# Optimization experiments

Measured on AMD Instinct MI355X. Metric: run time of the kernel, lower is better.

Reference implementation:

```python
import jax, jax.numpy as jnp
import numpy as np

B, T, H = 16, 2048, 1024

def setup_inputs() -> dict:
    key = jax.random.key(0)
    k1, k2, k3, k4 = jax.random.split(key, 4)
    stdv = 1.0 / np.sqrt(H)
    return {
        "hidden": jax.random.normal(k1, (B, H), dtype=jnp.float32),
        "encoder_outputs": jax.random.normal(k2, (B, T, 2 * H), dtype=jnp.float32),
        "W": jax.random.normal(k3, (H, 3 * H), dtype=jnp.float32) * stdv,  # nn.Linear(3H, H) weight
        "b": jnp.zeros((H,), dtype=jnp.float32),
        "v": jax.random.normal(k4, (H,), dtype=jnp.float32) * stdv,
    }

def reference(hidden, encoder_outputs, W, b, v):
    # hidden: (B,H); encoder_outputs: (B,T,2H)
    Bsz, Tlen, _ = encoder_outputs.shape
    Hrep = jnp.broadcast_to(hidden[:, None, :], (Bsz, Tlen, hidden.shape[-1]))  # (B,T,H)
    cat = jnp.concatenate([Hrep, encoder_outputs], axis=2)                      # (B,T,3H)
    energy = jnp.tanh(jnp.einsum('btk,hk->bth', cat, W) + b)                    # (B,T,H)
    scores = jnp.einsum('bth,h->bt', energy, v)[:, None, :]                     # (B,1,T), == bmm(v, energy^T)
    return jax.nn.softmax(scores, axis=2)
```

## Files before the change

### kernel.cpp

```cpp
#include <hip/hip_runtime.h>
#include <cstdint>

#define B_SZ 16
#define T_SZ 2048
#define H_SZ 1024
#define K_SZ 2048
#define M_SZ (B_SZ * T_SZ)

#define BM 128
#define BN 128
#define BK 64
#define LDK 72
#define KTILES (K_SZ / BK)

#define FBM 64
#define FBK 64

typedef _Float16 half8_t __attribute__((ext_vector_type(8)));
typedef _Float16 half4_t __attribute__((ext_vector_type(4)));
typedef float float4_t __attribute__((ext_vector_type(4)));

__global__ __launch_bounds__(256) void cvt_w2_kernel(
    const float* __restrict__ W, _Float16* __restrict__ dst) {
    int idx8 = blockIdx.x * 256 + threadIdx.x;
    int n = idx8 >> 8, k = (idx8 & 255) * 8;
    const float* src = W + (size_t)n * 3072 + H_SZ + k;
    float4_t a = *(const float4_t*)(src);
    float4_t b = *(const float4_t*)(src + 4);
    half8_t h;
    h[0] = (_Float16)a[0]; h[1] = (_Float16)a[1];
    h[2] = (_Float16)a[2]; h[3] = (_Float16)a[3];
    h[4] = (_Float16)b[0]; h[5] = (_Float16)b[1];
    h[6] = (_Float16)b[2]; h[7] = (_Float16)b[3];
    int nblk = n >> 4, m16 = n & 15;
    int kblk = k >> 5, quad = (k >> 3) & 3;
    size_t di = (((size_t)nblk * 64 + kblk) * 64 + quad * 16 + m16) * 8;
    *(half8_t*)(dst + di) = h;
}

__global__ __launch_bounds__(256) void hpart_kernel(
    const float* __restrict__ hidden, const float* __restrict__ W,
    const float* __restrict__ bias, float* __restrict__ hpart) {
    int wave = (blockIdx.x * 256 + threadIdx.x) >> 6;
    int lane = threadIdx.x & 63;
    int b = wave >> 10;
    int h = wave & 1023;
    const float* wrow = W + (size_t)h * 3072;
    const float* hrow = hidden + b * H_SZ;
    int k0 = lane * 16;
    float acc = 0.f;
#pragma unroll
    for (int j = 0; j < 4; ++j) {
        float4_t wv = *(const float4_t*)(wrow + k0 + j * 4);
        float4_t hv = *(const float4_t*)(hrow + k0 + j * 4);
        acc += wv[0] * hv[0] + wv[1] * hv[1] + wv[2] * hv[2] + wv[3] * hv[3];
    }
#pragma unroll
    for (int off = 32; off >= 1; off >>= 1) acc += __shfl_xor(acc, off, 64);
    if (lane == 0) hpart[b * H_SZ + h] = acc + bias[h];
}

__global__ __launch_bounds__(1024) void fused_attn_kernel(
    const float* __restrict__ enc, const _Float16* __restrict__ Bp,
    const float* __restrict__ hpart, const float* __restrict__ v,
    float* __restrict__ scores) {
    __shared__ __align__(16) _Float16 Af[2][FBM * FBK];
    __shared__ float hp_s[H_SZ];
    __shared__ float v_s[H_SZ];
    __shared__ float sred[8][FBM];

    const int tid = threadIdx.x;
    const int lane = tid & 63;
    const int w = tid >> 6;
    const int wn = w & 7;
    const int wmg = w >> 3;
    const int m16 = lane & 15, quad = lane >> 4;

    const int blockM = blockIdx.x;
    const int batch = blockM >> 5;

    hp_s[tid] = hpart[batch * H_SZ + tid];
    v_s[tid] = v[tid];

    float4_t acc[2][8];
#pragma unroll
    for (int i = 0; i < 2; ++i)
#pragma unroll
        for (int j = 0; j < 8; ++j) acc[i][j] = (float4_t){0.f, 0.f, 0.f, 0.f};

    const int arow = tid >> 4;
    const int acq = tid & 15;
    const float* Aptr = enc + (size_t)(blockM * FBM + arow) * K_SZ + acq * 4;
    const int wbyte = arow * 128 + ((((acq >> 1) ^ (arow & 7)) << 4) | ((acq & 1) * 8));
    char* AfB = (char*)Af;

    int fb[2][2];
#pragma unroll
    for (int tm = 0; tm < 2; ++tm) {
        int r = wmg * 32 + tm * 16 + m16;
#pragma unroll
        for (int ks = 0; ks < 2; ++ks)
            fb[tm][ks] = r * 128 + (((ks * 4 + quad) ^ (r & 7)) << 4);
    }

    const _Float16* Bfr = Bp + ((size_t)(wn * 8) * 64 * 64 + lane) * 8;

    {
        float4_t av = *(const float4_t*)(Aptr);
        half4_t h;
        h[0] = (_Float16)av[0]; h[1] = (_Float16)av[1];
        h[2] = (_Float16)av[2]; h[3] = (_Float16)av[3];
        *(half4_t*)(AfB + wbyte) = h;
    }
    __syncthreads();

    int cur = 0;
    for (int kt = 0; kt < K_SZ / FBK; ++kt) {
        float4_t av;
        if (kt < K_SZ / FBK - 1) av = *(const float4_t*)(Aptr + (kt + 1) * FBK);
#pragma unroll
        for (int ks = 0; ks < 2; ++ks) {
            half8_t af0 = *(const half8_t*)(AfB + cur * 8192 + fb[0][ks]);
            half8_t af1 = *(const half8_t*)(AfB + cur * 8192 + fb[1][ks]);
            const _Float16* bk = Bfr + (size_t)(kt * 2 + ks) * 512;
#pragma unroll
            for (int g = 0; g < 2; ++g) {
                half8_t bf0 = *(const half8_t*)(bk + (size_t)(g * 4 + 0) * 32768);
                half8_t bf1 = *(const half8_t*)(bk + (size_t)(g * 4 + 1) * 32768);
                half8_t bf2 = *(const half8_t*)(bk + (size_t)(g * 4 + 2) * 32768);
                half8_t bf3 = *(const half8_t*)(bk + (size_t)(g * 4 + 3) * 32768);
                __builtin_amdgcn_s_setprio(1);
                acc[0][g * 4 + 0] = __builtin_amdgcn_mfma_f32_16x16x32_f16(af0, bf0, acc[0][g * 4 + 0], 0, 0, 0);
                acc[1][g * 4 + 0] = __builtin_amdgcn_mfma_f32_16x16x32_f16(af1, bf0, acc[1][g * 4 + 0], 0, 0, 0);
                acc[0][g * 4 + 1] = __builtin_amdgcn_mfma_f32_16x16x32_f16(af0, bf1, acc[0][g * 4 + 1], 0, 0, 0);
                acc[1][g * 4 + 1] = __builtin_amdgcn_mfma_f32_16x16x32_f16(af1, bf1, acc[1][g * 4 + 1], 0, 0, 0);
                acc[0][g * 4 + 2] = __builtin_amdgcn_mfma_f32_16x16x32_f16(af0, bf2, acc[0][g * 4 + 2], 0, 0, 0);
                acc[1][g * 4 + 2] = __builtin_amdgcn_mfma_f32_16x16x32_f16(af1, bf2, acc[1][g * 4 + 2], 0, 0, 0);
                acc[0][g * 4 + 3] = __builtin_amdgcn_mfma_f32_16x16x32_f16(af0, bf3, acc[0][g * 4 + 3], 0, 0, 0);
                acc[1][g * 4 + 3] = __builtin_amdgcn_mfma_f32_16x16x32_f16(af1, bf3, acc[1][g * 4 + 3], 0, 0, 0);
                __builtin_amdgcn_s_setprio(0);
            }
        }
        if (kt < K_SZ / FBK - 1) {
            half4_t h;
            h[0] = (_Float16)av[0]; h[1] = (_Float16)av[1];
            h[2] = (_Float16)av[2]; h[3] = (_Float16)av[3];
            *(half4_t*)(AfB + (cur ^ 1) * 8192 + wbyte) = h;
        }
        __syncthreads();
        cur ^= 1;
    }

#pragma unroll
    for (int tm = 0; tm < 2; ++tm) {
        float s0 = 0.f, s1 = 0.f, s2 = 0.f, s3 = 0.f;
#pragma unroll
        for (int tn = 0; tn < 8; ++tn) {
            int nl = wn * 128 + tn * 16 + m16;
            float hpv = hp_s[nl];
            float vv = v_s[nl];
            s0 += tanhf(acc[tm][tn][0] + hpv) * vv;
            s1 += tanhf(acc[tm][tn][1] + hpv) * vv;
            s2 += tanhf(acc[tm][tn][2] + hpv) * vv;
            s3 += tanhf(acc[tm][tn][3] + hpv) * vv;
        }
#pragma unroll
        for (int off = 1; off < 16; off <<= 1) {
            s0 += __shfl_xor(s0, off, 64);
            s1 += __shfl_xor(s1, off, 64);
            s2 += __shfl_xor(s2, off, 64);
            s3 += __shfl_xor(s3, off, 64);
        }
        if (m16 == 0) {
            int rl = wmg * 32 + tm * 16 + quad * 4;
            sred[wn][rl + 0] = s0;
            sred[wn][rl + 1] = s1;
            sred[wn][rl + 2] = s2;
            sred[wn][rl + 3] = s3;
        }
    }
    __syncthreads();
    if (tid < FBM) {
        float t = 0.f;
#pragma unroll
        for (int i = 0; i < 8; ++i) t += sred[i][tid];
        scores[(size_t)blockM * FBM + tid] = t;
    }
}

__global__ __launch_bounds__(256) void softmax1_kernel(
    const float* __restrict__ scores, float* __restrict__ out) {
    __shared__ float red[256];
    const int b = blockIdx.x;
    const int tid = threadIdx.x;
    float sc[8];
    float mymax = -1e30f;
#pragma unroll
    for (int i = 0; i < 8; ++i) {
        float s = scores[b * T_SZ + i * 256 + tid];
        sc[i] = s;
        mymax = fmaxf(mymax, s);
    }
    red[tid] = mymax;
    __syncthreads();
    for (int off = 128; off >= 1; off >>= 1) {
        if (tid < off) red[tid] = fmaxf(red[tid], red[tid + off]);
        __syncthreads();
    }
    float mx = red[0];
    __syncthreads();
    float mysum = 0.f;
#pragma unroll
    for (int i = 0; i < 8; ++i) {
        sc[i] = expf(sc[i] - mx);
        mysum += sc[i];
    }
    red[tid] = mysum;
    __syncthreads();
    for (int off = 128; off >= 1; off >>= 1) {
        if (tid < off) red[tid] += red[tid + off];
        __syncthreads();
    }
    float inv = 1.0f / red[0];
#pragma unroll
    for (int i = 0; i < 8; ++i) out[b * T_SZ + i * 256 + tid] = sc[i] * inv;
}

__global__ __launch_bounds__(256, 2) void attn_gemm_kernel(
    const float* __restrict__ enc, const float* __restrict__ W,
    const float* __restrict__ hpart, const float* __restrict__ v,
    float* __restrict__ partial) {
    __shared__ _Float16 Afs[BM * LDK];
    __shared__ _Float16 Bfs[BN * LDK];
    __shared__ float hp_s[BN];
    __shared__ float v_s[BN];

    const int bidx = blockIdx.x;
    const int blockN = bidx & 7;
    const int blockM = bidx >> 3;
    const int tid = threadIdx.x;
    const int lane = tid & 63;
    const int w = tid >> 6;
    const int wm = w & 1, wn = w >> 1;
    const int m16 = lane & 15, quad = lane >> 4;

    const int n0 = blockN * BN;
    const int batch = blockM >> 4;

    if (tid < BN) {
        hp_s[tid] = hpart[batch * H_SZ + n0 + tid];
        v_s[tid] = v[n0 + tid];
    }

    float4_t acc[4][4];
#pragma unroll
    for (int i = 0; i < 4; ++i)
#pragma unroll
        for (int j = 0; j < 4; ++j) acc[i][j] = (float4_t){0.f, 0.f, 0.f, 0.f};

    const float* Abase = enc + (size_t)(blockM * BM) * K_SZ;
    const float* Bbase = W + (size_t)n0 * 3072 + H_SZ;

    for (int kt = 0; kt < KTILES; ++kt) {
        __syncthreads();
        const float* Asrc0 = Abase + kt * BK;
#pragma unroll
        for (int i = 0; i < 4; ++i) {
            int f8 = i * 256 + tid;
            int r = f8 >> 3, c8 = f8 & 7;
            const float* src = Asrc0 + (size_t)r * K_SZ + c8 * 8;
            float4_t lo = *(const float4_t*)(src);
            float4_t hi = *(const float4_t*)(src + 4);
            half8_t hv;
            hv[0] = (_Float16)lo[0]; hv[1] = (_Float16)lo[1];
            hv[2] = (_Float16)lo[2]; hv[3] = (_Float16)lo[3];
            hv[4] = (_Float16)hi[0]; hv[5] = (_Float16)hi[1];
            hv[6] = (_Float16)hi[2]; hv[7] = (_Float16)hi[3];
            *(half8_t*)&Afs[r * LDK + c8 * 8] = hv;
        }
        const float* Bsrc0 = Bbase + kt * BK;
#pragma unroll
        for (int i = 0; i < 4; ++i) {
            int f8 = i * 256 + tid;
            int r = f8 >> 3, c8 = f8 & 7;
            const float* src = Bsrc0 + (size_t)r * 3072 + c8 * 8;
            float4_t lo = *(const float4_t*)(src);
            float4_t hi = *(const float4_t*)(src + 4);
            half8_t hv;
            hv[0] = (_Float16)lo[0]; hv[1] = (_Float16)lo[1];
            hv[2] = (_Float16)lo[2]; hv[3] = (_Float16)lo[3];
            hv[4] = (_Float16)hi[0]; hv[5] = (_Float16)hi[1];
            hv[6] = (_Float16)hi[2]; hv[7] = (_Float16)hi[3];
            *(half8_t*)&Bfs[r * LDK + c8 * 8] = hv;
        }
        __syncthreads();
#pragma unroll
        for (int ks = 0; ks < 2; ++ks) {
            half8_t afrag[4], bfrag[4];
#pragma unroll
            for (int tm = 0; tm < 4; ++tm)
                afrag[tm] = *(const half8_t*)&Afs[(wm * 64 + tm * 16 + m16) * LDK + ks * 32 + quad * 8];
#pragma unroll
            for (int tn = 0; tn < 4; ++tn)
                bfrag[tn] = *(const half8_t*)&Bfs[(wn * 64 + tn * 16 + m16) * LDK + ks * 32 + quad * 8];
#pragma unroll
            for (int tm = 0; tm < 4; ++tm)
#pragma unroll
                for (int tn = 0; tn < 4; ++tn)
                    acc[tm][tn] = __builtin_amdgcn_mfma_f32_16x16x32_f16(
                        afrag[tm], bfrag[tn], acc[tm][tn], 0, 0, 0);
        }
    }

    const int slice = blockN * 2 + wn;
#pragma unroll
    for (int tm = 0; tm < 4; ++tm) {
        float s0 = 0.f, s1 = 0.f, s2 = 0.f, s3 = 0.f;
#pragma unroll
        for (int tn = 0; tn < 4; ++tn) {
            int nl = wn * 64 + tn * 16 + m16;
            float hpv = hp_s[nl];
            float vv = v_s[nl];
            s0 += tanhf(acc[tm][tn][0] + hpv) * vv;
            s1 += tanhf(acc[tm][tn][1] + hpv) * vv;
            s2 += tanhf(acc[tm][tn][2] + hpv) * vv;
            s3 += tanhf(acc[tm][tn][3] + hpv) * vv;
        }
#pragma unroll
        for (int off = 1; off < 16; off <<= 1) {
            s0 += __shfl_xor(s0, off, 64);
            s1 += __shfl_xor(s1, off, 64);
            s2 += __shfl_xor(s2, off, 64);
            s3 += __shfl_xor(s3, off, 64);
        }
        if (m16 == 0) {
            int gm = blockM * BM + wm * 64 + tm * 16 + quad * 4;
            float* dst = partial + (size_t)slice * M_SZ + gm;
            dst[0] = s0; dst[1] = s1; dst[2] = s2; dst[3] = s3;
        }
    }
}

__global__ __launch_bounds__(256) void softmax_kernel(
    const float* __restrict__ partial, float* __restrict__ out) {
    __shared__ float red[256];
    const int b = blockIdx.x;
    const int tid = threadIdx.x;
    float sc[8];
    float mymax = -1e30f;
#pragma unroll
    for (int i = 0; i < 8; ++i) {
        int t = i * 256 + tid;
        float s = 0.f;
#pragma unroll
        for (int sl = 0; sl < 16; ++sl) s += partial[(size_t)sl * M_SZ + b * T_SZ + t];
        sc[i] = s;
        mymax = fmaxf(mymax, s);
    }
    red[tid] = mymax;
    __syncthreads();
    for (int off = 128; off >= 1; off >>= 1) {
        if (tid < off) red[tid] = fmaxf(red[tid], red[tid + off]);
        __syncthreads();
    }
    float mx = red[0];
    __syncthreads();
    float mysum = 0.f;
#pragma unroll
    for (int i = 0; i < 8; ++i) {
        sc[i] = expf(sc[i] - mx);
        mysum += sc[i];
    }
    red[tid] = mysum;
    __syncthreads();
    for (int off = 128; off >= 1; off >>= 1) {
        if (tid < off) red[tid] += red[tid + off];
        __syncthreads();
    }
    float inv = 1.0f / red[0];
#pragma unroll
    for (int i = 0; i < 8; ++i) out[b * T_SZ + i * 256 + tid] = sc[i] * inv;
}

extern "C" void kernel_launch(void* const* d_in, const int* in_sizes, int n_in,
                              void* d_out, int out_size, void* d_ws, size_t ws_size,
                              hipStream_t stream) {
    const float* hidden = (const float*)d_in[0];
    const float* enc    = (const float*)d_in[1];
    const float* W      = (const float*)d_in[2];
    const float* bias   = (const float*)d_in[3];
    const float* v      = (const float*)d_in[4];
    float* out = (float*)d_out;

    float* hpart  = (float*)d_ws;
    float* scores = hpart + B_SZ * H_SZ;
    _Float16* w2h = (_Float16*)(scores + M_SZ);
    const size_t need = (size_t)((char*)(w2h + (size_t)H_SZ * K_SZ) - (char*)d_ws);

    hipLaunchKernelGGL(hpart_kernel, dim3(4096), dim3(256), 0, stream,
                       hidden, W, bias, hpart);
    if (ws_size >= need) {
        hipLaunchKernelGGL(cvt_w2_kernel, dim3(1024), dim3(256), 0, stream, W, w2h);
        hipLaunchKernelGGL(fused_attn_kernel, dim3(M_SZ / FBM), dim3(1024), 0, stream,
                           enc, w2h, hpart, v, scores);
        hipLaunchKernelGGL(softmax1_kernel, dim3(B_SZ), dim3(256), 0, stream,
                           scores, out);
    } else {
        float* partial = scores;
        hipLaunchKernelGGL(attn_gemm_kernel, dim3(2048), dim3(256), 0, stream,
                           enc, W, hpart, v, partial);
        hipLaunchKernelGGL(softmax_kernel, dim3(B_SZ), dim3(256), 0, stream,
                           partial, out);
    }
}
```

Before: 556.4 us.

## Stage W tiles in LDS via direct global-to-LDS loads with 512-thread blocks

The fused GEMM kernel now uses 512 threads (8 waves), and each wave computes a 64x128 tile instead of 32x128. Pre-converted fp16 W fragments are staged into double-buffered LDS with global_load_lds, replacing per-wave direct global loads. The K step shrinks to 32, and encoder rows are read with nontemporal loads. The aim is to cut redundant global/L2 traffic for W and to raise MFMA density per fragment load, at the cost of 128KB of LDS, more accumulator registers, and one barrier per smaller K step.

```diff
diff --git a/kernel.cpp b/kernel.cpp
--- a/kernel.cpp
+++ b/kernel.cpp
@@ -14,11 +14,18 @@
 #define KTILES (K_SZ / BK)
 
 #define FBM 64
-#define FBK 64
+#define FBK 32
+#define NSTEPS (K_SZ / FBK)
 
 typedef _Float16 half8_t __attribute__((ext_vector_type(8)));
 typedef _Float16 half4_t __attribute__((ext_vector_type(4)));
 typedef float float4_t __attribute__((ext_vector_type(4)));
+
+__device__ __forceinline__ void glds16(const _Float16* g, _Float16* l) {
+    __builtin_amdgcn_global_load_lds(
+        (const __attribute__((address_space(1))) void*)g,
+        (__attribute__((address_space(3))) void*)l, 16, 0, 0);
+}
 
 __global__ __launch_bounds__(256) void cvt_w2_kernel(
     const float* __restrict__ W, _Float16* __restrict__ dst) {
@@ -60,109 +67,112 @@
     if (lane == 0) hpart[b * H_SZ + h] = acc + bias[h];
 }
 
-__global__ __launch_bounds__(1024) void fused_attn_kernel(
+__global__ __launch_bounds__(512, 2) void fused2_attn_kernel(
     const float* __restrict__ enc, const _Float16* __restrict__ Bp,
     const float* __restrict__ hpart, const float* __restrict__ v,
     float* __restrict__ scores) {
-    __shared__ __align__(16) _Float16 Af[2][FBM * FBK];
-    __shared__ float hp_s[H_SZ];
-    __shared__ float v_s[H_SZ];
-    __shared__ float sred[8][FBM];
+    __shared__ __align__(16) _Float16 Als[2][FBM * FBK];
+    __shared__ __align__(16) _Float16 Bls[2][64 * 512];
 
     const int tid = threadIdx.x;
     const int lane = tid & 63;
     const int w = tid >> 6;
-    const int wn = w & 7;
-    const int wmg = w >> 3;
     const int m16 = lane & 15, quad = lane >> 4;
 
     const int blockM = blockIdx.x;
     const int batch = blockM >> 5;
 
-    hp_s[tid] = hpart[batch * H_SZ + tid];
-    v_s[tid] = v[tid];
-
-    float4_t acc[2][8];
-#pragma unroll
-    for (int i = 0; i < 2; ++i)
+    const int arow = tid >> 3;
+    const int ac8 = tid & 7;
+    const float* Ap = enc + (size_t)(blockM * FBM + arow) * K_SZ + ac8 * 4;
+    const int awbyte = arow * 64 +
+        ((((ac8 >> 1) ^ ((arow >> 1) & 3)) << 4) | ((ac8 & 1) << 3));
+
+    int afb[4];
+#pragma unroll
+    for (int tm = 0; tm < 4; ++tm) {
+        int r = tm * 16 + m16;
+        afb[tm] = r * 64 + ((quad ^ ((r >> 1) & 3)) << 4);
+    }
+
+    const _Float16* Bg = Bp + ((size_t)(w * 8) * 64) * 512 + lane * 8;
+
+    float4_t acc[4][8];
+#pragma unroll
+    for (int i = 0; i < 4; ++i)
 #pragma unroll
         for (int j = 0; j < 8; ++j) acc[i][j] = (float4_t){0.f, 0.f, 0.f, 0.f};
 
-    const int arow = tid >> 4;
-    const int acq = tid & 15;
-    const float* Aptr = enc + (size_t)(blockM * FBM + arow) * K_SZ + acq * 4;
-    const int wbyte = arow * 128 + ((((acq >> 1) ^ (arow & 7)) << 4) | ((acq & 1) * 8));
-    char* AfB = (char*)Af;
-
-    int fb[2][2];
-#pragma unroll
-    for (int tm = 0; tm < 2; ++tm) {
-        int r = wmg * 32 + tm * 16 + m16;
-#pragma unroll
-        for (int ks = 0; ks < 2; ++ks)
-            fb[tm][ks] = r * 128 + (((ks * 4 + quad) ^ (r & 7)) << 4);
-    }
-
-    const _Float16* Bfr = Bp + ((size_t)(wn * 8) * 64 * 64 + lane) * 8;
-
     {
-        float4_t av = *(const float4_t*)(Aptr);
+        float4_t av = __builtin_nontemporal_load((const float4_t*)Ap);
+#pragma unroll
+        for (int i = 0; i < 8; ++i)
+            glds16(Bg + (size_t)i * (64 * 512), &Bls[0][(w * 8 + i) * 512]);
         half4_t h;
         h[0] = (_Float16)av[0]; h[1] = (_Float16)av[1];
         h[2] = (_Float16)av[2]; h[3] = (_Float16)av[3];
-        *(half4_t*)(AfB + wbyte) = h;
+        *(half4_t*)((char*)Als[0] + awbyte) = h;
     }
     __syncthreads();
 
     int cur = 0;
-    for (int kt = 0; kt < K_SZ / FBK; ++kt) {
+    for (int kt = 0; kt < NSTEPS; ++kt) {
+        const bool pre = (kt + 1 < NSTEPS);
         float4_t av;
-        if (kt < K_SZ / FBK - 1) av = *(const float4_t*)(Aptr + (kt + 1) * FBK);
-#pragma unroll
-        for (int ks = 0; ks < 2; ++ks) {
-            half8_t af0 = *(const half8_t*)(AfB + cur * 8192 + fb[0][ks]);
-            half8_t af1 = *(const half8_t*)(AfB + cur * 8192 + fb[1][ks]);
-            const _Float16* bk = Bfr + (size_t)(kt * 2 + ks) * 512;
-#pragma unroll
-            for (int g = 0; g < 2; ++g) {
-                half8_t bf0 = *(const half8_t*)(bk + (size_t)(g * 4 + 0) * 32768);
-                half8_t bf1 = *(const half8_t*)(bk + (size_t)(g * 4 + 1) * 32768);
-                half8_t bf2 = *(const half8_t*)(bk + (size_t)(g * 4 + 2) * 32768);
-                half8_t bf3 = *(const half8_t*)(bk + (size_t)(g * 4 + 3) * 32768);
-                __builtin_amdgcn_s_setprio(1);
-                acc[0][g * 4 + 0] = __builtin_amdgcn_mfma_f32_16x16x32_f16(af0, bf0, acc[0][g * 4 + 0], 0, 0, 0);
-                acc[1][g * 4 + 0] = __builtin_amdgcn_mfma_f32_16x16x32_f16(af1, bf0, acc[1][g * 4 + 0], 0, 0, 0);
-                acc[0][g * 4 + 1] = __builtin_amdgcn_mfma_f32_16x16x32_f16(af0, bf1, acc[0][g * 4 + 1], 0, 0, 0);
-                acc[1][g * 4 + 1] = __builtin_amdgcn_mfma_f32_16x16x32_f16(af1, bf1, acc[1][g * 4 + 1], 0, 0, 0);
-                acc[0][g * 4 + 2] = __builtin_amdgcn_mfma_f32_16x16x32_f16(af0, bf2, acc[0][g * 4 + 2], 0, 0, 0);
-                acc[1][g * 4 + 2] = __builtin_amdgcn_mfma_f32_16x16x32_f16(af1, bf2, acc[1][g * 4 + 2], 0, 0, 0);
-                acc[0][g * 4 + 3] = __builtin_amdgcn_mfma_f32_16x16x32_f16(af0, bf3, acc[0][g * 4 + 3], 0, 0, 0);
-                acc[1][g * 4 + 3] = __builtin_amdgcn_mfma_f32_16x16x32_f16(af1, bf3, acc[1][g * 4 + 3], 0, 0, 0);
-                __builtin_amdgcn_s_setprio(0);
-            }
-        }
-        if (kt < K_SZ / FBK - 1) {
+        if (pre) {
+            av = __builtin_nontemporal_load(
+                (const float4_t*)(Ap + (size_t)(kt + 1) * FBK));
+#pragma unroll
+            for (int i = 0; i < 8; ++i)
+                glds16(Bg + (size_t)i * (64 * 512) + (size_t)(kt + 1) * 512,
+                       &Bls[cur ^ 1][(w * 8 + i) * 512]);
+        }
+        half8_t af[4], bf[8];
+#pragma unroll
+        for (int tm = 0; tm < 4; ++tm)
+            af[tm] = *(const half8_t*)((const char*)Als[cur] + afb[tm]);
+#pragma unroll
+        for (int tn = 0; tn < 8; ++tn)
+            bf[tn] = *(const half8_t*)&Bls[cur][(w * 8 + tn) * 512 + lane * 8];
+
+        __builtin_amdgcn_s_setprio(1);
+#pragma unroll
+        for (int tm = 0; tm < 4; ++tm)
+#pragma unroll
+            for (int tn = 0; tn < 8; ++tn)
+                acc[tm][tn] = __builtin_amdgcn_mfma_f32_16x16x32_f16(
+                    af[tm], bf[tn], acc[tm][tn], 0, 0, 0);
+        __builtin_amdgcn_s_setprio(0);
+
+        if (pre) {
             half4_t h;
             h[0] = (_Float16)av[0]; h[1] = (_Float16)av[1];
             h[2] = (_Float16)av[2]; h[3] = (_Float16)av[3];
-            *(half4_t*)(AfB + (cur ^ 1) * 8192 + wbyte) = h;
+            *(half4_t*)((char*)Als[cur ^ 1] + awbyte) = h;
         }
         __syncthreads();
         cur ^= 1;
     }
 
-#pragma unroll
-    for (int tm = 0; tm < 2; ++tm) {
+    float* sred = (float*)Als;
+
+    float hpv[8], vv[8];
+#pragma unroll
+    for (int tn = 0; tn < 8; ++tn) {
+        int col = w * 128 + tn * 16 + m16;
+        hpv[tn] = hpart[batch * H_SZ + col];
+        vv[tn] = v[col];
+    }
+
+#pragma unroll
+    for (int tm = 0; tm < 4; ++tm) {
         float s0 = 0.f, s1 = 0.f, s2 = 0.f, s3 = 0.f;
 #pragma unroll
         for (int tn = 0; tn < 8; ++tn) {
-            int nl = wn * 128 + tn * 16 + m16;
-            float hpv = hp_s[nl];
-            float vv = v_s[nl];
-            s0 += tanhf(acc[tm][tn][0] + hpv) * vv;
-            s1 += tanhf(acc[tm][tn][1] + hpv) * vv;
-            s2 += tanhf(acc[tm][tn][2] + hpv) * vv;
-            s3 += tanhf(acc[tm][tn][3] + hpv) * vv;
+            s0 += tanhf(acc[tm][tn][0] + hpv[tn]) * vv[tn];
+            s1 += tanhf(acc[tm][tn][1] + hpv[tn]) * vv[tn];
+            s2 += tanhf(acc[tm][tn][2] + hpv[tn]) * vv[tn];
+            s3 += tanhf(acc[tm][tn][3] + hpv[tn]) * vv[tn];
         }
 #pragma unroll
         for (int off = 1; off < 16; off <<= 1) {
@@ -172,18 +182,18 @@
             s3 += __shfl_xor(s3, off, 64);
         }
         if (m16 == 0) {
-            int rl = wmg * 32 + tm * 16 + quad * 4;
-            sred[wn][rl + 0] = s0;
-            sred[wn][rl + 1] = s1;
-            sred[wn][rl + 2] = s2;
-            sred[wn][rl + 3] = s3;
+            int rl = tm * 16 + quad * 4;
+            sred[w * 64 + rl + 0] = s0;
+            sred[w * 64 + rl + 1] = s1;
+            sred[w * 64 + rl + 2] = s2;
+            sred[w * 64 + rl + 3] = s3;
         }
     }
     __syncthreads();
     if (tid < FBM) {
         float t = 0.f;
 #pragma unroll
-        for (int i = 0; i < 8; ++i) t += sred[i][tid];
+        for (int i = 0; i < 8; ++i) t += sred[i * 64 + tid];
         scores[(size_t)blockM * FBM + tid] = t;
     }
 }
@@ -401,7 +411,7 @@
                        hidden, W, bias, hpart);
     if (ws_size >= need) {
         hipLaunchKernelGGL(cvt_w2_kernel, dim3(1024), dim3(256), 0, stream, W, w2h);
-        hipLaunchKernelGGL(fused_attn_kernel, dim3(M_SZ / FBM), dim3(1024), 0, stream,
+        hipLaunchKernelGGL(fused2_attn_kernel, dim3(M_SZ / FBM), dim3(512), 0, stream,
                            enc, w2h, hpart, v, scores);
         hipLaunchKernelGGL(softmax1_kernel, dim3(B_SZ), dim3(256), 0, stream,
                            scores, out);
```

Result: slower. 572.2 us (+2.8%).
